# Performance work log

Hardware: AMD Instinct MI355X
Metric: run time of the kernel (lower is better)

## Reference

```python
import jax, jax.numpy as jnp
import numpy as np

N1 = 8000   # solute nodes
N2 = 8000   # solvent nodes
E = 128000  # edges per graph side (avg degree 16)
B = 128     # number of graphs in the batch
NFEAT, NHID, NCLS = 128, 256, 512
D = 2 * NCLS   # Set2Set input dim (1024)
H = D          # LSTM hidden = input_dim in DGL Set2Set


def setup_inputs() -> dict:
    key = jax.random.key(0)
    ks = jax.random.split(key, 24)
    w = lambda k, shp, fan: (jax.random.normal(k, shp, jnp.float32) / np.sqrt(fan))
    inp = {}
    inp["x1"] = jax.random.normal(ks[0], (N1, NFEAT), jnp.float32)
    inp["x2"] = jax.random.normal(ks[1], (N2, NFEAT), jnp.float32)
    inp["src1"] = jax.random.randint(ks[2], (E,), 0, N1, jnp.int32)
    inp["dst1"] = jax.random.randint(ks[3], (E,), 0, N1, jnp.int32)
    inp["src2"] = jax.random.randint(ks[4], (E,), 0, N2, jnp.int32)
    inp["dst2"] = jax.random.randint(ks[5], (E,), 0, N2, jnp.int32)
    inp["gid1"] = jnp.sort(jax.random.randint(ks[6], (N1,), 0, B, jnp.int32))
    inp["gid2"] = jnp.sort(jax.random.randint(ks[7], (N2,), 0, B, jnp.int32))
    # GraphConv weights (DGL stores W as [in, out]) + biases
    inp["W_gc1"] = w(ks[8], (NFEAT, NHID), NFEAT); inp["b_gc1"] = jnp.zeros((NHID,), jnp.float32)
    inp["W_gc2"] = w(ks[9], (NHID, NCLS), NHID);   inp["b_gc2"] = jnp.zeros((NCLS,), jnp.float32)
    inp["W_gc3"] = w(ks[10], (NFEAT, NHID), NFEAT); inp["b_gc3"] = jnp.zeros((NHID,), jnp.float32)
    inp["W_gc4"] = w(ks[11], (NHID, NCLS), NHID);   inp["b_gc4"] = jnp.zeros((NCLS,), jnp.float32)
    # Set2Set LSTM (input = 2*D, hidden = H), torch gate order i,f,g,o
    inp["W_ih"] = w(ks[12], (4 * H, 2 * D), 2 * D)
    inp["W_hh"] = w(ks[13], (4 * H, H), H)
    inp["b_ih"] = jnp.zeros((4 * H,), jnp.float32)
    inp["b_hh"] = jnp.zeros((4 * H,), jnp.float32)
    # MLP head
    inp["W_fc1"] = w(ks[14], (1024, 4096), 4096); inp["b_fc1"] = jnp.zeros((1024,), jnp.float32)
    inp["W_fc2"] = w(ks[15], (512, 1024), 1024);  inp["b_fc2"] = jnp.zeros((512,), jnp.float32)
    inp["W_fc3"] = w(ks[16], (1, 512), 512);      inp["b_fc3"] = jnp.zeros((1,), jnp.float32)
    return inp


def _gconv(x, src, dst, W, b, n):
    # DGL GraphConv, norm='both': D_out^{-1/2} scaling at src, sum over in-edges, D_in^{-1/2} at dst
    ones = jnp.ones(src.shape[0], x.dtype)
    outd = jnp.clip(jax.ops.segment_sum(ones, src, num_segments=n), 1.0)
    ind = jnp.clip(jax.ops.segment_sum(ones, dst, num_segments=n), 1.0)
    h = (x * (outd ** -0.5)[:, None]) @ W
    agg = jax.ops.segment_sum(h[src], dst, num_segments=n)   # sparse neighbor aggregation
    return agg * (ind ** -0.5)[:, None] + b


def _set2set(x, gid, Wih, Whh, bih, bhh):
    # DGL Set2Set, n_iters=2, 1-layer LSTM; x: [N, D], gid: [N] graph membership
    d = x.shape[1]
    q_star = jnp.zeros((B, 2 * d), x.dtype)
    h = jnp.zeros((B, d), x.dtype)
    c = jnp.zeros((B, d), x.dtype)
    for _ in range(2):
        gates = q_star @ Wih.T + h @ Whh.T + bih + bhh
        i, f, g, o = jnp.split(gates, 4, axis=1)
        c = jax.nn.sigmoid(f) * c + jax.nn.sigmoid(i) * jnp.tanh(g)
        h = jax.nn.sigmoid(o) * jnp.tanh(c)
        e = jnp.sum(x * h[gid], axis=1)                       # per-node attention logit
        m = jax.ops.segment_max(e, gid, num_segments=B)
        ex = jnp.exp(e - m[gid])
        s = jax.ops.segment_sum(ex, gid, num_segments=B)
        alpha = ex / s[gid]                                   # segment softmax
        r = jax.ops.segment_sum(alpha[:, None] * x, gid, num_segments=B)
        q_star = jnp.concatenate([h, r], axis=1)
    return q_star


def reference(x1, x2, src1, dst1, src2, dst2, gid1, gid2,
              W_gc1, b_gc1, W_gc2, b_gc2, W_gc3, b_gc3, W_gc4, b_gc4,
              W_ih, W_hh, b_ih, b_hh,
              W_fc1, b_fc1, W_fc2, b_fc2, W_fc3, b_fc3):
    s = jax.nn.relu(_gconv(x1, src1, dst1, W_gc1, b_gc1, N1))
    s = _gconv(s, src1, dst1, W_gc2, b_gc2, N1)
    v = jax.nn.relu(_gconv(x2, src2, dst2, W_gc3, b_gc3, N2))
    v = _gconv(v, src2, dst2, W_gc4, b_gc4, N2)
    # len_map = len1.T @ len2 == same-graph indicator for binary membership matrices
    len_map = (gid1[:, None] == gid2[None, :]).astype(s.dtype)
    imap = jnp.tanh(s @ v.T) * len_map                        # [N1, N2]
    solvent_prime = imap.T @ s                                # [N2, NCLS]
    solute_prime = imap @ v                                   # [N1, NCLS]
    sf = jnp.concatenate([s, solute_prime], axis=1)           # [N1, 2*NCLS]
    vf = jnp.concatenate([v, solvent_prime], axis=1)
    ss = _set2set(sf, gid1, W_ih, W_hh, b_ih, b_hh)           # [B, 4*NCLS]
    vs = _set2set(vf, gid2, W_ih, W_hh, b_ih, b_hh)
    z = jnp.concatenate([ss, vs], axis=1)                     # [B, 4096]
    z = jax.nn.relu(z @ W_fc1.T + b_fc1)
    z = jax.nn.relu(z @ W_fc2.T + b_fc2)
    return z @ W_fc3.T + b_fc3                                # [B, 1]
```

## Files before the change

### kernel.cpp

```cpp
#include <hip/hip_runtime.h>

#define DEV __device__ __forceinline__

typedef _Float16 half8 __attribute__((ext_vector_type(8)));
typedef _Float16 half4_t __attribute__((ext_vector_type(4)));
typedef float f32x4 __attribute__((ext_vector_type(4)));

DEV float ftanh(float x){
  float ax = fabsf(x);
  float e = __expf(-2.f*ax);
  float t = (1.f - e)/(1.f + e);
  return x < 0.f ? -t : t;
}
DEV float fsigm(float x){ return 1.f/(1.f + expf(-x)); }
DEV float wredsum(float v){
  #pragma unroll
  for (int o=32;o;o>>=1) v += __shfl_xor(v,o,64);
  return v;
}
DEV f32x4 MF(half8 a, half8 b, f32x4 c){
  return __builtin_amdgcn_mfma_f32_16x16x32_f16(a,b,c,0,0,0);
}
DEV void split8(float4 a0, float4 a1, half8& h, half8& l){
  float f[8] = {a0.x,a0.y,a0.z,a0.w,a1.x,a1.y,a1.z,a1.w};
  #pragma unroll
  for (int e=0;e<8;++e){
    _Float16 hh = (_Float16)f[e];
    h[e] = hh;
    l[e] = (_Float16)(f[e] - (float)hh);
  }
}

__global__ void k_zero_i32(int* __restrict__ p, int n){
  int i = blockIdx.x*256 + threadIdx.x; if (i<n) p[i]=0;
}

__global__ void k_hist2(const int* __restrict__ s1, const int* __restrict__ d1, int E1,
                        int* __restrict__ co1, int* __restrict__ ci1,
                        const int* __restrict__ s2, const int* __restrict__ d2, int E2,
                        int* __restrict__ co2, int* __restrict__ ci2){
  int e = blockIdx.x*256 + threadIdx.x;
  if (e < E1){ atomicAdd(&co1[s1[e]],1); atomicAdd(&ci1[d1[e]],1); }
  int f = e - E1;
  if (f >= 0 && f < E2){ atomicAdd(&co2[s2[f]],1); atomicAdd(&ci2[d2[f]],1); }
}

__global__ void k_scan2(const int* __restrict__ c1, int n1, int* __restrict__ r1,
                        const int* __restrict__ c2, int n2, int* __restrict__ r2){
  __shared__ int sm[1024];
  const int* cnt = blockIdx.x ? c2 : c1;
  int*       row = blockIdx.x ? r2 : r1;
  int n          = blockIdx.x ? n2 : n1;
  int t = threadIdx.x;
  int per = n/1024 + 1;
  int st = t*per;
  int s = 0;
  for (int i=st;i<st+per;++i) if (i<n) s += cnt[i];
  sm[t]=s; __syncthreads();
  for (int o=1;o<1024;o<<=1){
    int v = (t>=o)? sm[t-o]:0;
    __syncthreads();
    sm[t] += v;
    __syncthreads();
  }
  int base = sm[t]-s;
  for (int i=st;i<st+per;++i){
    if (i<=n) row[i]=base;
    if (i<n) base += cnt[i];
  }
}

__global__ void k_scale2(const int* __restrict__ co1, const int* __restrict__ ci1, int n1,
                         float* __restrict__ os1, float* __restrict__ is1,
                         const int* __restrict__ co2, const int* __restrict__ ci2, int n2,
                         float* __restrict__ os2, float* __restrict__ is2){
  int i = blockIdx.x*256+threadIdx.x;
  if (i<n1){
    int a = co1[i] > 1 ? co1[i] : 1;
    int b = ci1[i] > 1 ? ci1[i] : 1;
    os1[i] = 1.f/sqrtf((float)a);
    is1[i] = 1.f/sqrtf((float)b);
  }
  int j = i - n1;
  if (j>=0 && j<n2){
    int a = co2[j] > 1 ? co2[j] : 1;
    int b = ci2[j] > 1 ? ci2[j] : 1;
    os2[j] = 1.f/sqrtf((float)a);
    is2[j] = 1.f/sqrtf((float)b);
  }
}

__global__ void k_scatter2(const int* __restrict__ s1, const int* __restrict__ d1, int E1,
                           const int* __restrict__ row1, int* __restrict__ cur1, int* __restrict__ csr1,
                           const int* __restrict__ s2, const int* __restrict__ d2, int E2,
                           const int* __restrict__ row2, int* __restrict__ cur2, int* __restrict__ csr2){
  int e = blockIdx.x*256+threadIdx.x;
  if (e<E1){ int d=d1[e]; int p=atomicAdd(&cur1[d],1); csr1[row1[d]+p]=s1[e]; }
  int f = e - E1;
  if (f>=0 && f<E2){ int d=d2[f]; int p=atomicAdd(&cur2[d],1); csr2[row2[d]+p]=s2[f]; }
}

__global__ void k_goff2(const int* __restrict__ g1, int n1, int* __restrict__ o1,
                        const int* __restrict__ g2, int n2, int* __restrict__ o2, int B,
                        int* __restrict__ pb1, int* __restrict__ gm1,
                        int* __restrict__ pb2, int* __restrict__ gm2){
  __shared__ int sc[2][256];
  int t = threadIdx.x;
  const int* gid = (t>=256)? g2 : g1;
  int*      goff = (t>=256)? o2 : o1;
  int n          = (t>=256)? n2 : n1;
  const int side = t>>8, q = t & 255;
  if (q<=B){
    int lo=0, hi=n;
    while (lo<hi){ int mid=(lo+hi)>>1; if (gid[mid]<q) lo=mid+1; else hi=mid; }
    goff[q]=lo;
  }
  __syncthreads();
  int pc = 0;
  if (q < B){
    const int* go = side ? o2 : o1;
    int c = go[q+1]-go[q]; if (c>128) c=128;
    pc = (c+31)&~31;
  }
  sc[side][q] = pc;
  __syncthreads();
  for (int o=1;o<B;o<<=1){
    int v = (q>=o && q<B) ? sc[side][q-o] : 0;
    __syncthreads();
    if (q<B) sc[side][q] += v;
    __syncthreads();
  }
  if (q < B){
    int incl = sc[side][q];
    int pbv  = incl - pc;
    int* pb = side ? pb2 : pb1;
    int* gm = side ? gm2 : gm1;
    pb[q] = pbv;
    if (q == B-1) pb[B] = incl;
    int nb = pc>>5, b0 = pbv>>5;
    for (int k=0;k<nb;++k) gm[b0+k] = q;
  }
}

__global__ void k_agg_h(const float* __restrict__ x, int ldx, const float* __restrict__ osc,
                        const int* __restrict__ row, const int* __restrict__ csr,
                        _Float16* __restrict__ oh, _Float16* __restrict__ ol, int n, int f4shift){
  int F4 = 1<<f4shift;
  int node = blockIdx.x*(256>>f4shift) + (threadIdx.x>>f4shift);
  if (node>=n) return;
  int fc = threadIdx.x & (F4-1);
  int F = F4<<2;
  int rs=row[node], re=row[node+1];
  float ax=0, ay=0, az=0, aw=0;
  if (osc){
    for (int e=rs;e<re;++e){
      int s = csr[e];
      float sc = osc[s];
      const float4 v = *(const float4*)(x + (size_t)s*ldx + (fc<<2));
      ax += sc*v.x; ay += sc*v.y; az += sc*v.z; aw += sc*v.w;
    }
  } else {
    int e = rs;
    for (; e+1<re; e+=2){
      int s0 = csr[e], s1 = csr[e+1];
      const float4 v0 = *(const float4*)(x + (size_t)s0*ldx + (fc<<2));
      const float4 v1 = *(const float4*)(x + (size_t)s1*ldx + (fc<<2));
      ax += v0.x+v1.x; ay += v0.y+v1.y; az += v0.z+v1.z; aw += v0.w+v1.w;
    }
    if (e<re){
      int s0 = csr[e];
      const float4 v0 = *(const float4*)(x + (size_t)s0*ldx + (fc<<2));
      ax += v0.x; ay += v0.y; az += v0.z; aw += v0.w;
    }
  }
  half4_t hv, lv;
  hv.x = (_Float16)ax; lv.x = (_Float16)(ax - (float)hv.x);
  hv.y = (_Float16)ay; lv.y = (_Float16)(ay - (float)hv.y);
  hv.z = (_Float16)az; lv.z = (_Float16)(az - (float)hv.z);
  hv.w = (_Float16)aw; lv.w = (_Float16)(aw - (float)hv.w);
  size_t o = (size_t)node*F + (fc<<2);
  *(half4_t*)(oh + o) = hv;
  *(half4_t*)(ol + o) = lv;
}

__global__ void k_wpack4(const float* __restrict__ W0, const float* __restrict__ W1,
                         const float* __restrict__ W2, const float* __restrict__ W3,
                         _Float16* __restrict__ h0, _Float16* __restrict__ l0,
                         _Float16* __restrict__ h1, _Float16* __restrict__ l1,
                         _Float16* __restrict__ h2, _Float16* __restrict__ l2,
                         _Float16* __restrict__ h3, _Float16* __restrict__ l3){
  int w = blockIdx.y;
  const float* W = (w==0)?W0:(w==1)?W1:(w==2)?W2:W3;
  _Float16* oh = (w==0)?h0:(w==1)?h1:(w==2)?h2:h3;
  _Float16* ol = (w==0)?l0:(w==1)?l1:(w==2)?l2:l3;
  int K   = (w&1)? 256 : 128;
  int nsh = (w&1)? 9 : 8;
  int i = blockIdx.x*256 + threadIdx.x;
  if (i >= (K<<nsh)) return;
  int k = i >> nsh, n = i & ((1<<nsh)-1);
  float v = W[i];
  _Float16 h = (_Float16)v;
  _Float16 l = (_Float16)(v - (float)h);
  size_t p = (((size_t)(k>>3)<<nsh) + n)*8 + (k&7);
  oh[p] = h; ol[p] = l;
}

__global__ __launch_bounds__(256)
void k_wpackT(const float* __restrict__ W, int ldw, int N,
              _Float16* __restrict__ Bh, _Float16* __restrict__ Bl){
  __shared__ float st[32][260];
  const int k0 = (int)blockIdx.x << 8;
  const int n0 = (int)blockIdx.y << 5;
  const int t = threadIdx.x;
  const int r = t >> 3, la = t & 7;
  const float* src = W + (size_t)(n0 + r)*ldw + k0;
  #pragma unroll
  for (int q=0;q<8;++q){
    int f = (la<<2) + (q<<5);
    *(float4*)&st[r][f] = *(const float4*)(src + f);
  }
  __syncthreads();
  const int nl = t & 31;
  #pragma unroll
  for (int j=0;j<4;++j){
    int kbl = (t>>5) + (j<<3);
    half8 h8, l8;
    #pragma unroll
    for (int e=0;e<8;++e){
      float v = st[nl][(kbl<<3)+e];
      _Float16 hh = (_Float16)v;
      h8[e]=hh; l8[e]=(_Float16)(v-(float)hh);
    }
    size_t a = ((size_t)((k0>>3)+kbl)*N + n0 + nl)*8;
    *(half8*)(Bh + a) = h8;
    *(half8*)(Bl + a) = l8;
  }
}

__global__ __launch_bounds__(256)
void k_gconv_mfma(const _Float16* __restrict__ Ah0, const _Float16* __restrict__ Al0,
                  const _Float16* __restrict__ Ah1, const _Float16* __restrict__ Al1,
                  const _Float16* __restrict__ Bh0, const _Float16* __restrict__ Bl0,
                  const _Float16* __restrict__ Bh1, const _Float16* __restrict__ Bl1,
                  float* __restrict__ C0, float* __restrict__ C1, int ldc,
                  int M0, int M1, int N, int K,
                  const float* __restrict__ rs0, const float* __restrict__ rs1,
                  const float* __restrict__ bi0, const float* __restrict__ bi1, int relu,
                  const float* __restrict__ po0, const float* __restrict__ po1)
{
  __shared__ __align__(16) _Float16 Ahs[2][4096];
  __shared__ __align__(16) _Float16 Als[2][4096];

  const int gx = gridDim.x, gxy = gridDim.x*gridDim.y;
  const int nwg = gxy*2;
  int fid = blockIdx.x + gx*blockIdx.y + gxy*blockIdx.z;
  int q = nwg>>3, r = nwg&7;
  int xcd = fid & 7, idx = fid >> 3;
  int sid = (xcd<r ? xcd*(q+1) : r*(q+1)+(xcd-r)*q) + idx;
  const int z  = sid / gxy;  int rem = sid - z*gxy;
  const int by = rem / gx,  bx = rem - by*gx;

  const _Float16* Ah = z ? Ah1 : Ah0;
  const _Float16* Al = z ? Al1 : Al0;
  const _Float16* Bh = z ? Bh1 : Bh0;
  const _Float16* Bl = z ? Bl1 : Bl0;
  float*       C  = z ? C1 : C0;
  const float* rsc = z ? rs1 : rs0;
  const float* bia = z ? bi1 : bi0;
  const float* po  = z ? po1 : po0;
  const int M = z ? M1 : M0;

  const int row0 = by << 7;
  const int col0 = bx << 7;
  if (row0 >= ((M+127)&~127)) return;

  const int tid = threadIdx.x;
  const int am  = tid >> 2;
  const int akb = tid & 3;
  const int wid = tid >> 6, lane = tid & 63;
  const int wr = wid >> 1, wc = wid & 1;
  const int lr = lane & 15, lg = lane >> 4;

  f32x4 acc[4][4] = {};
  const int nt = K >> 5;
  const size_t rowK64 = (size_t)64 * K;
  const _Float16* Aph = Ah + (size_t)(row0 + am) * K + (akb<<3);
  const _Float16* Apl = Al + (size_t)(row0 + am) * K + (akb<<3);

  half8 gh0 = *(const half8*)(Aph);
  half8 gh1 = *(const half8*)(Aph + rowK64);
  half8 gl0 = *(const half8*)(Apl);
  half8 gl1 = *(const half8*)(Apl + rowK64);
  *(half8*)&Ahs[0][(akb*128 + am)*8]      = gh0;
  *(half8*)&Ahs[0][(akb*128 + am + 64)*8] = gh1;
  *(half8*)&Als[0][(akb*128 + am)*8]      = gl0;
  *(half8*)&Als[0][(akb*128 + am + 64)*8] = gl1;
  __syncthreads();

  for (int c = 0; c < nt; ++c){
    const int cb = c & 1;
    if (c + 1 < nt){
      const int k0 = (c + 1) << 5;
      gh0 = *(const half8*)(Aph + k0);
      gh1 = *(const half8*)(Aph + k0 + rowK64);
      gl0 = *(const half8*)(Apl + k0);
      gl1 = *(const half8*)(Apl + k0 + rowK64);
    }
    const size_t kb0 = (size_t)(c<<2) + lg;
    half8 bh[4], bl[4];
    #pragma unroll
    for (int ni=0;ni<4;++ni){
      size_t a = (kb0*N + col0 + (wc<<6) + (ni<<4) + lr)*8;
      bh[ni] = *(const half8*)(Bh + a);
      bl[ni] = *(const half8*)(Bl + a);
    }
    #pragma unroll
    for (int mi=0;mi<4;++mi){
      const int aa = ((lg<<7) + (wr<<6) + (mi<<4) + lr)<<3;
      half8 ah = *(const half8*)&Ahs[cb][aa];
      half8 al = *(const half8*)&Als[cb][aa];
      #pragma unroll
      for (int ni=0;ni<4;++ni){
        acc[mi][ni] = MF(ah, bh[ni], acc[mi][ni]);
        acc[mi][ni] = MF(al, bh[ni], acc[mi][ni]);
        acc[mi][ni] = MF(ah, bl[ni], acc[mi][ni]);
      }
    }
    if (c + 1 < nt){
      const int nb_ = cb ^ 1;
      *(half8*)&Ahs[nb_][(akb*128 + am)*8]      = gh0;
      *(half8*)&Ahs[nb_][(akb*128 + am + 64)*8] = gh1;
      *(half8*)&Als[nb_][(akb*128 + am)*8]      = gl0;
      *(half8*)&Als[nb_][(akb*128 + am + 64)*8] = gl1;
    }
    __syncthreads();
  }

  #pragma unroll
  for (int ni = 0; ni < 4; ++ni){
    int cc = col0 + (wc<<6) + (ni<<4) + lr;
    float bv = bia ? bia[cc] : 0.f;
    #pragma unroll
    for (int mi = 0; mi < 4; ++mi){
      int rbase = row0 + (wr<<6) + (mi<<4) + (lg<<2);
      #pragma unroll
      for (int j = 0; j < 4; ++j){
        int rr = rbase + j;
        if (rr < M){
          float rs_ = rsc ? rsc[rr] : 1.f;
          float v = acc[mi][ni][j]*rs_ + bv;
          if (relu) v = fmaxf(v, 0.f);
          if (po) v *= po[rr];
          C[(size_t)rr*ldc + cc] = v;
        }
      }
    }
  }
}

__global__ __launch_bounds__(256)
void k_pack(const float* __restrict__ sf, const float* __restrict__ vf,
            const int* __restrict__ go1, const int* __restrict__ go2,
            const int* __restrict__ pb1, const int* __restrict__ pb2,
            const int* __restrict__ gm1, const int* __restrict__ gm2,
            _Float16* __restrict__ p1h, _Float16* __restrict__ p1l,
            _Float16* __restrict__ p2h, _Float16* __restrict__ p2l, int B)
{
  __shared__ float st[32][516];
  const int side = blockIdx.y;
  const float* x = side ? vf : sf;
  const int* go = side ? go2 : go1;
  const int* pb = side ? pb2 : pb1;
  const int* gm = side ? gm2 : gm1;
  _Float16* ph = side ? p2h : p1h;
  _Float16* pl = side ? p2l : p1l;
  const int u = blockIdx.x;
  if (u*32 >= pb[B]) return;
  const int g = gm[u];
  const int j0 = u*32 - pb[g];
  const int base = go[g];
  int cnt = go[g+1]-base; if (cnt>128) cnt=128;
  const int t = threadIdx.x;
  const int r = t>>3, f0 = (t&7)<<2;
  const bool valid = (j0 + r) < cnt;
  const float* src = x + (size_t)(base + j0 + r)*1024;
  #pragma unroll
  for (int q=0;q<16;++q){
    int f = f0 + (q<<5);
    float4 vv;
    if (valid) vv = *(const float4*)(src + f);
    else { vv.x=0.f; vv.y=0.f; vv.z=0.f; vv.w=0.f; }
    *(float4*)&st[r][f] = vv;
  }
  __syncthreads();
  #pragma unroll
  for (int q=0;q<8;++q){
    int u2 = t + (q<<8);
    int jg = u2>>9, f = u2&511;
    half8 h8, l8;
    #pragma unroll
    for (int e=0;e<8;++e){
      float vvv = st[(jg<<3)+e][f];
      _Float16 hh = (_Float16)vvv;
      h8[e]=hh; l8[e]=(_Float16)(vvv-(float)hh);
    }
    size_t a = ((size_t)((u<<2)+jg)<<12) + ((size_t)f<<3);
    *(half8*)(ph + a) = h8;
    *(half8*)(pl + a) = l8;
  }
}

__global__ __launch_bounds__(256)
void k_T(const float* __restrict__ sf, const float* __restrict__ vf,
         const int* __restrict__ go1, const int* __restrict__ go2,
         _Float16* __restrict__ Th, _Float16* __restrict__ Tl, int B)
{
  __shared__ __align__(16) _Float16 Ahs[64*136 + 8];
  __shared__ __align__(16) _Float16 Als[64*136 + 8];
  __shared__ __align__(16) _Float16 Bhs[2][2048];
  __shared__ __align__(16) _Float16 Bls[2][2048];
  const int g = blockIdx.x, rt = blockIdx.y;
  int gR = go1[g]; int c1 = go1[g+1]-gR; if (c1>128) c1=128;
  int gO = go2[g]; int c2 = go2[g+1]-gO; if (c2>128) c2=128;
  const int c1_32 = (c1+31)&~31, c2_32 = (c2+31)&~31;
  if ((rt<<4) >= c1_32 || c2_32 == 0) return;
  const int tid = threadIdx.x;
  {
    const int r = tid >> 4;
    const int f0 = (tid & 15) << 5;
    const int row = (rt<<4) + r;
    const bool val = row < c1;
    const float* src = sf + (size_t)(gR + row)*1024 + f0;
    #pragma unroll
    for (int q=0;q<4;++q){
      float4 v0, v1;
      if (val){
        v0 = *(const float4*)(src + (q<<3));
        v1 = *(const float4*)(src + (q<<3) + 4);
      } else {
        v0.x=0.f; v0.y=0.f; v0.z=0.f; v0.w=0.f; v1 = v0;
      }
      half8 h,l; split8(v0,v1,h,l);
      const int a = ((f0>>3) + q)*136 + (r<<3);
      *(half8*)&Ahs[a] = h; *(half8*)&Als[a] = l;
    }
  }
  const int w = tid>>6, lane = tid&63, lr = lane&15, lg = lane>>4;
  const int bc = tid>>2, bfg = tid&3, bf = bfg<<3;
  const int bwr = (bfg<<9) + ((bc ^ (bfg<<2))<<3);
  const int ncc = (c2_32 + 63) >> 6;
  _Float16* T0h = Th + ((size_t)g<<14);
  _Float16* T0l = Tl + ((size_t)g<<14);
  _Float16* T1h = Th + ((size_t)(B + g)<<14);
  _Float16* T1l = Tl + ((size_t)(B + g)<<14);
  for (int cc=0; cc<ncc; ++cc){
    const int cbase = cc<<6;
    const int colr = cbase + bc;
    const bool bval = colr < c2;
    const float* bsrc = vf + (size_t)(gO + colr)*1024 + bf;
    {
      float4 v0, v1;
      if (bval){ v0 = *(const float4*)(bsrc); v1 = *(const float4*)(bsrc + 4); }
      else { v0.x=0.f; v0.y=0.f; v0.z=0.f; v0.w=0.f; v1 = v0; }
      half8 h,l; split8(v0,v1,h,l);
      *(half8*)&Bhs[0][bwr] = h; *(half8*)&Bls[0][bwr] = l;
    }
    __syncthreads();
    f32x4 acc = {0.f,0.f,0.f,0.f};
    const int col_l = (w<<4) + lr;
    const int ba = (lg<<9) + ((col_l ^ (lg<<2))<<3);
    for (int kc=0; kc<16; ++kc){
      float4 p0, p1;
      if (kc+1<16){
        if (bval){
          const float* s = bsrc + ((kc+1)<<5);
          p0 = *(const float4*)s; p1 = *(const float4*)(s + 4);
        } else { p0.x=0.f; p0.y=0.f; p0.z=0.f; p0.w=0.f; p1 = p0; }
      }
      const int aa = ((kc<<2)+lg)*136 + (lr<<3);
      half8 ah = *(const half8*)&Ahs[aa];
      half8 al = *(const half8*)&Als[aa];
      half8 bh = *(const half8*)&Bhs[kc&1][ba];
      half8 bl = *(const half8*)&Bls[kc&1][ba];
      acc = MF(ah,bh,acc);
      acc = MF(al,bh,acc);
      acc = MF(ah,bl,acc);
      if (kc+1<16){
        half8 h,l; split8(p0,p1,h,l);
        *(half8*)&Bhs[(kc+1)&1][bwr] = h; *(half8*)&Bls[(kc+1)&1][bwr] = l;
      }
      __syncthreads();
    }
    const int col = cbase + col_l;
    if (col < c2_32){
      half4_t t1h, t1l;
      #pragma unroll
      for (int qq=0;qq<4;++qq){
        int r = (rt<<4) + (lg<<2) + qq;
        float t = (r < c1 && col < c2) ? ftanh(acc[qq]) : 0.f;
        _Float16 hh = (_Float16)t;
        _Float16 ll = (_Float16)(t - (float)hh);
        T0h[(r<<7) + col] = hh;
        T0l[(r<<7) + col] = ll;
        t1h[qq] = hh; t1l[qq] = ll;
      }
      const int r0 = (rt<<4) + (lg<<2);
      *(half4_t*)&T1h[(col<<7) + r0] = t1h;
      *(half4_t*)&T1l[(col<<7) + r0] = t1l;
    }
  }
}

__global__ __launch_bounds__(256)
void k_apply(const _Float16* __restrict__ Th, const _Float16* __restrict__ Tl,
             const _Float16* __restrict__ p1h, const _Float16* __restrict__ p1l,
             const _Float16* __restrict__ p2h, const _Float16* __restrict__ p2l,
             const int* __restrict__ go1, const int* __restrict__ go2,
             const int* __restrict__ pb1, const int* __restrict__ pb2,
             float* __restrict__ sf, float* __restrict__ vf, int B)
{
  const int side = blockIdx.x, g = blockIdx.y, ft = blockIdx.z;
  const int* goR = side ? go2 : go1;
  const int* goO = side ? go1 : go2;
  const int* pbO = side ? pb1 : pb2;
  const _Float16* oph = side ? p1h : p2h;
  const _Float16* opl = side ? p1l : p2l;
  float* outp = side ? vf : sf;
  int gR = goR[g]; int cR = goR[g+1]-gR; if (cR>128) cR=128;
  int gO = goO[g]; int cO = goO[g+1]-gO; if (cO>128) cO=128;
  if (cR <= 0) return;
  const int pO = pbO[g];
  const int cO32 = (cO+31)&~31;
  const int MR = ((cR+15)&~15)>>4;
  const _Float16* Tph = Th + ((size_t)(side*B + g)<<14);
  const _Float16* Tpl = Tl + ((size_t)(side*B + g)<<14);
  const int tid = threadIdx.x, w = tid>>6, lane = tid&63;
  const int lr = lane&15, lg = lane>>4;
  const int f0 = (ft<<8) + (w<<6);
  for (int rc = 0; rc < MR; rc += 4){
    f32x4 acc[4][4];
    #pragma unroll
    for (int a_=0;a_<4;++a_)
      #pragma unroll
      for (int b_=0;b_<4;++b_) acc[a_][b_] = (f32x4){0.f,0.f,0.f,0.f};
    for (int k0=0; k0<cO32; k0+=32){
      half8 bh[4], bl[4];
      #pragma unroll
      for (int nj=0;nj<4;++nj){
        size_t a = ((size_t)((pO + k0)>>3) + lg)*4096 + (size_t)(f0 + (nj<<4) + lr)*8;
        bh[nj] = *(const half8*)(oph + a);
        bl[nj] = *(const half8*)(opl + a);
      }
      #pragma unroll
      for (int mi=0;mi<4;++mi){
        if (rc + mi < MR){
          int a = ((((rc+mi)<<4) + lr)<<7) + k0 + (lg<<3);
          half8 th_ = *(const half8*)&Tph[a];
          half8 tl_ = *(const half8*)&Tpl[a];
          #pragma unroll
          for (int nj=0;nj<4;++nj){
            acc[mi][nj] = MF(th_, bh[nj], acc[mi][nj]);
            acc[mi][nj] = MF(tl_, bh[nj], acc[mi][nj]);
            acc[mi][nj] = MF(th_, bl[nj], acc[mi][nj]);
          }
        }
      }
    }
    #pragma unroll
    for (int mi=0;mi<4;++mi){
      if (rc + mi < MR){
        #pragma unroll
        for (int nj=0;nj<4;++nj){
          #pragma unroll
          for (int qq=0;qq<4;++qq){
            int r = (((rc+mi)<<4)) + (lg<<2) + qq;
            if (r < cR)
              outp[(size_t)(gR + r)*1024 + 512 + f0 + (nj<<4) + lr] = acc[mi][nj][qq];
          }
        }
      }
    }
  }
}

__global__ __launch_bounds__(256)
void k_gemmsk(const float* __restrict__ Ab, size_t AsideOff, int lda,
              const float* __restrict__ Bm, int ldb,
              float* __restrict__ P, int M, int N, int kchunk)
{
  __shared__ float As[2][16][132];
  __shared__ float Bs[2][16][68];
  const int tid = threadIdx.x;
  const int col0 = (int)blockIdx.x << 6;
  const int kbeg = (int)blockIdx.z * kchunk;
  const float* A = Ab + (size_t)blockIdx.y * AsideOff;
  const int ar = tid >> 1, ak = (tid & 1) << 3;
  const int br = tid >> 2, bk = (tid & 3) << 2;
  const int tx = tid & 15, ty = tid >> 4;
  const float* Arow = A + (size_t)ar * lda + kbeg + ak;
  const float* Brow = Bm + (size_t)(col0 + br) * ldb + kbeg + bk;
  float acc[8][4] = {};
  float4 a0 = *(const float4*)(Arow);
  float4 a1 = *(const float4*)(Arow + 4);
  float4 b0 = *(const float4*)(Brow);
  As[0][ak+0][ar]=a0.x; As[0][ak+1][ar]=a0.y; As[0][ak+2][ar]=a0.z; As[0][ak+3][ar]=a0.w;
  As[0][ak+4][ar]=a1.x; As[0][ak+5][ar]=a1.y; As[0][ak+6][ar]=a1.z; As[0][ak+7][ar]=a1.w;
  Bs[0][bk+0][br]=b0.x; Bs[0][bk+1][br]=b0.y; Bs[0][bk+2][br]=b0.z; Bs[0][bk+3][br]=b0.w;
  __syncthreads();
  const int nt = kchunk >> 4;
  for (int t = 0; t < nt; ++t){
    const int cb = t & 1;
    if (t + 1 < nt){
      int k0 = (t + 1) << 4;
      a0 = *(const float4*)(Arow + k0);
      a1 = *(const float4*)(Arow + k0 + 4);
      b0 = *(const float4*)(Brow + k0);
    }
    #pragma unroll
    for (int kk = 0; kk < 16; ++kk){
      float4 b4 = *(const float4*)&Bs[cb][kk][tx << 2];
      float4 a4 = *(const float4*)&As[cb][kk][ty << 3];
      float4 a5 = *(const float4*)&As[cb][kk][(ty << 3) + 4];
      acc[0][0]+=a4.x*b4.x; acc[0][1]+=a4.x*b4.y; acc[0][2]+=a4.x*b4.z; acc[0][3]+=a4.x*b4.w;
      acc[1][0]+=a4.y*b4.x; acc[1][1]+=a4.y*b4.y; acc[1][2]+=a4.y*b4.z; acc[1][3]+=a4.y*b4.w;
      acc[2][0]+=a4.z*b4.x; acc[2][1]+=a4.z*b4.y; acc[2][2]+=a4.z*b4.z; acc[2][3]+=a4.z*b4.w;
      acc[3][0]+=a4.w*b4.x; acc[3][1]+=a4.w*b4.y; acc[3][2]+=a4.w*b4.z; acc[3][3]+=a4.w*b4.w;
      acc[4][0]+=a5.x*b4.x; acc[4][1]+=a5.x*b4.y; acc[4][2]+=a5.x*b4.z; acc[4][3]+=a5.x*b4.w;
      acc[5][0]+=a5.y*b4.x; acc[5][1]+=a5.y*b4.y; acc[5][2]+=a5.y*b4.z; acc[5][3]+=a5.y*b4.w;
      acc[6][0]+=a5.z*b4.x; acc[6][1]+=a5.z*b4.y; acc[6][2]+=a5.z*b4.z; acc[6][3]+=a5.z*b4.w;
      acc[7][0]+=a5.w*b4.x; acc[7][1]+=a5.w*b4.y; acc[7][2]+=a5.w*b4.z; acc[7][3]+=a5.w*b4.w;
    }
    if (t + 1 < nt){
      const int nb = cb ^ 1;
      As[nb][ak+0][ar]=a0.x; As[nb][ak+1][ar]=a0.y; As[nb][ak+2][ar]=a0.z; As[nb][ak+3][ar]=a0.w;
      As[nb][ak+4][ar]=a1.x; As[nb][ak+5][ar]=a1.y; As[nb][ak+6][ar]=a1.z; As[nb][ak+7][ar]=a1.w;
      Bs[nb][bk+0][br]=b0.x; Bs[nb][bk+1][br]=b0.y; Bs[nb][bk+2][br]=b0.z; Bs[nb][bk+3][br]=b0.w;
    }
    __syncthreads();
  }
  float* Pz = P + (size_t)(blockIdx.y*gridDim.z + blockIdx.z) * M * N;
  #pragma unroll
  for (int i = 0; i < 8; ++i){
    int rr = (ty << 3) + i;
    float4 v = {acc[i][0], acc[i][1], acc[i][2], acc[i][3]};
    *(float4*)(Pz + (size_t)rr*N + col0 + (tx<<2)) = v;
  }
}

__global__ __launch_bounds__(256)
void k_gemmsk_h(const float* __restrict__ Ab, size_t AsideOff, int lda,
                const _Float16* __restrict__ Bhp, const _Float16* __restrict__ Blp,
                float* __restrict__ P, int N, int kchunk)
{
  __shared__ __align__(16) _Float16 Ahs[2][4096];
  __shared__ __align__(16) _Float16 Als[2][4096];
  const int tid = threadIdx.x;
  const int col0 = (int)blockIdx.x << 7;
  const int kbeg = (int)blockIdx.z * kchunk;
  const float* A = Ab + (size_t)blockIdx.y * AsideOff;
  const int ar = tid >> 1, aq = (tid & 1) << 4;
  const int wid = tid>>6, lane = tid&63;
  const int wr = wid>>1, wc = wid&1;
  const int lr = lane&15, lg = lane>>4;
  const float* Arow = A + (size_t)ar*lda + kbeg + aq;
  const int akb = aq>>3;
  f32x4 acc[4][4] = {};
  const int nc = kchunk >> 5;
  float4 g0,g1,g2,g3;
  g0 = *(const float4*)(Arow);     g1 = *(const float4*)(Arow+4);
  g2 = *(const float4*)(Arow+8);   g3 = *(const float4*)(Arow+12);
  {
    half8 h,l;
    split8(g0,g1,h,l);
    *(half8*)&Ahs[0][(akb*128+ar)*8] = h;     *(half8*)&Als[0][(akb*128+ar)*8] = l;
    split8(g2,g3,h,l);
    *(half8*)&Ahs[0][((akb+1)*128+ar)*8] = h; *(half8*)&Als[0][((akb+1)*128+ar)*8] = l;
  }
  __syncthreads();
  for (int c=0;c<nc;++c){
    const int cb = c&1;
    if (c+1<nc){
      const float* p = Arow + ((c+1)<<5);
      g0 = *(const float4*)(p);    g1 = *(const float4*)(p+4);
      g2 = *(const float4*)(p+8);  g3 = *(const float4*)(p+12);
    }
    const size_t kb0 = (size_t)((kbeg + (c<<5)) >> 3) + lg;
    half8 bh[4], bl[4];
    #pragma unroll
    for (int ni=0;ni<4;++ni){
      size_t a = (kb0*N + col0 + (wc<<6) + (ni<<4) + lr)*8;
      bh[ni] = *(const half8*)(Bhp + a);
      bl[ni] = *(const half8*)(Blp + a);
    }
    #pragma unroll
    for (int mi=0;mi<4;++mi){
      int aa = ((lg<<7) + (wr<<6) + (mi<<4) + lr)<<3;
      half8 ah = *(const half8*)&Ahs[cb][aa];
      half8 al = *(const half8*)&Als[cb][aa];
      #pragma unroll
      for (int ni=0;ni<4;++ni){
        acc[mi][ni] = MF(ah,bh[ni],acc[mi][ni]);
        acc[mi][ni] = MF(al,bh[ni],acc[mi][ni]);
        acc[mi][ni] = MF(ah,bl[ni],acc[mi][ni]);
      }
    }
    if (c+1<nc){
      const int nb = cb^1;
      half8 h,l;
      split8(g0,g1,h,l);
      *(half8*)&Ahs[nb][(akb*128+ar)*8] = h;     *(half8*)&Als[nb][(akb*128+ar)*8] = l;
      split8(g2,g3,h,l);
      *(half8*)&Ahs[nb][((akb+1)*128+ar)*8] = h; *(half8*)&Als[nb][((akb+1)*128+ar)*8] = l;
    }
    __syncthreads();
  }
  float* Pz = P + (size_t)(blockIdx.y*gridDim.z + blockIdx.z)*128*N;
  #pragma unroll
  for (int mi=0;mi<4;++mi){
    #pragma unroll
    for (int ni=0;ni<4;++ni){
      int cc2 = col0 + (wc<<6) + (ni<<4) + lr;
      #pragma unroll
      for (int j=0;j<4;++j){
        int rr2 = (wr<<6) + (mi<<4) + (lg<<2) + j;
        Pz[(size_t)rr2*N + cc2] = acc[mi][ni][j];
      }
    }
  }
}

__global__ void k_red_bias(const float* __restrict__ P, int split, int MN, int N,
                           const float* __restrict__ bias, float* __restrict__ C, int relu){
  int i = blockIdx.x*256 + threadIdx.x;
  if (i >= MN) return;
  float v = bias[i & (N-1)];
  for (int s=0;s<split;++s) v += P[(size_t)s*MN + i];
  if (relu) v = fmaxf(v, 0.f);
  C[i] = v;
}

__global__ void k_lstm1(const float* __restrict__ bih, const float* __restrict__ bhh,
                        float* __restrict__ c1, float* __restrict__ h1){
  int j = blockIdx.x*256 + threadIdx.x;
  if (j >= 1024) return;
  float gi = bih[j]        + bhh[j];
  float gg = bih[j+2048]   + bhh[j+2048];
  float go = bih[j+3072]   + bhh[j+3072];
  float cc = fsigm(gi)*ftanh(gg);
  c1[j] = cc;
  h1[j] = fsigm(go)*ftanh(cc);
}

__global__ void k_gemv_u(const float* __restrict__ Wih, const float* __restrict__ Whh,
                         const float* __restrict__ bih, const float* __restrict__ bhh,
                         const float* __restrict__ h1, float* __restrict__ u){
  int w = (blockIdx.x*256 + threadIdx.x)>>6;
  int lane = threadIdx.x & 63;
  if (w >= 4096) return;
  const float* wi = Wih + (size_t)w*2048;
  const float* wh = Whh + (size_t)w*1024;
  float acc = 0.f;
  #pragma unroll
  for (int qq=0;qq<4;++qq){
    int o = qq*256 + (lane<<2);
    float4 hv = *(const float4*)(h1 + o);
    float4 a  = *(const float4*)(wi + o);
    float4 b  = *(const float4*)(wh + o);
    acc += hv.x*(a.x+b.x) + hv.y*(a.y+b.y) + hv.z*(a.z+b.z) + hv.w*(a.w+b.w);
  }
  acc = wredsum(acc);
  if (lane==0) u[w] = acc + bih[w] + bhh[w];
}

__global__ __launch_bounds__(256)
void k_attn(const float* __restrict__ sf, const float* __restrict__ vf,
            const int* __restrict__ go1, const int* __restrict__ go2,
            const float* __restrict__ hbase, size_t hSideOff, int hstride,
            float* __restrict__ outbase, size_t oSideOff, int ldout)
{
  __shared__ float hs[1024];
  __shared__ float ech[1024];
  __shared__ float red[8];
  int side = blockIdx.y;
  const float* x = side? vf : sf;
  const int* goff = side? go2 : go1;
  const float* hsrc = hbase + (size_t)side*hSideOff;
  float* outp = outbase + (size_t)side*oSideOff;
  int b = blockIdx.x, t = threadIdx.x;
  int i0 = goff[b], i1 = goff[b+1];
  int lane = t & 63, wv = t >> 6;
  { float4 hv = *(const float4*)(hsrc + (size_t)b*hstride + (t<<2));
    *(float4*)&hs[t<<2] = hv; }
  __syncthreads();
  float m = -3.0e38f, s = 0.f;
  float ax=0, ay=0, az=0, aw=0;
  for (int c = i0; c < i1; c += 1024){
    int ce = c + 1024; if (ce > i1) ce = i1;
    int n = ce - c;
    float wmax = -3.0e38f;
    for (int i = c + wv; i < ce; i += 4){
      const float* xr = x + (size_t)i*1024;
      float d = 0.f;
      #pragma unroll
      for (int qq=0;qq<4;++qq){
        int o = qq*256 + (lane<<2);
        float4 xv = *(const float4*)(xr+o);
        float4 h4 = *(const float4*)&hs[o];
        d += xv.x*h4.x + xv.y*h4.y + xv.z*h4.z + xv.w*h4.w;
      }
      d = wredsum(d);
      if (lane==0) ech[i-c] = d;
      wmax = fmaxf(wmax, d);
    }
    if (lane==0) red[wv] = wmax;
    __syncthreads();
    float cm = fmaxf(fmaxf(red[0],red[1]), fmaxf(red[2],red[3]));
    float nm = fmaxf(m, cm);
    float scale = __expf(m - nm);
    s *= scale; ax*=scale; ay*=scale; az*=scale; aw*=scale;
    float ps = 0.f;
    for (int k = t; k < n; k += 256) ps += __expf(ech[k]-nm);
    ps = wredsum(ps);
    __syncthreads();
    if (lane==0) red[wv] = ps;
    __syncthreads();
    s += red[0]+red[1]+red[2]+red[3];
    for (int k = 0; k < n; ++k){
      float w = __expf(ech[k]-nm);
      float4 xv = *(const float4*)(x + (size_t)(c+k)*1024 + (t<<2));
      ax += w*xv.x; ay += w*xv.y; az += w*xv.z; aw += w*xv.w;
    }
    m = nm;
    __syncthreads();
  }
  float inv = (i1>i0 && s>0.f) ? 1.f/s : 0.f;
  float4 o = {ax*inv, ay*inv, az*inv, aw*inv};
  *(float4*)(outp + (size_t)b*ldout + (t<<2)) = o;
}

__global__ void k_lstm2_red(const float* __restrict__ Pb, size_t PsideOff, int split,
                            const float* __restrict__ u, const float* __restrict__ c1,
                            float* __restrict__ z, int B){
  int idx = blockIdx.x*256 + threadIdx.x;
  if (idx >= B*1024) return;
  int side = blockIdx.y;
  const float* P = Pb + (size_t)side*PsideOff;
  int b = idx >> 10, j = idx & 1023;
  float gi=u[j], gf=u[j+1024], gg=u[j+2048], go=u[j+3072];
  const float* g = P + (size_t)b*4096;
  for (int s=0;s<split;++s){
    const float* gs = g + (size_t)s*B*4096;
    gi += gs[j]; gf += gs[j+1024]; gg += gs[j+2048]; go += gs[j+3072];
  }
  float cc = fsigm(gf)*c1[j] + fsigm(gi)*ftanh(gg);
  z[(size_t)b*4096 + side*2048 + j] = fsigm(go)*ftanh(cc);
}

__global__ void k_fc3(const float* __restrict__ z2, const float* __restrict__ w3,
                      const float* __restrict__ b3, float* __restrict__ out, int B){
  int wv = (blockIdx.x*256+threadIdx.x)>>6;
  int lane = threadIdx.x & 63;
  if (wv >= B) return;
  const float* zr = z2 + (size_t)wv*512;
  float acc=0.f;
  #pragma unroll
  for (int qq=0;qq<2;++qq){
    int o = qq*256 + (lane<<2);
    float4 a  = *(const float4*)(zr + o);
    float4 ww = *(const float4*)(w3 + o);
    acc += a.x*ww.x + a.y*ww.y + a.z*ww.z + a.w*ww.w;
  }
  acc = wredsum(acc);
  if (lane==0) out[wv] = acc + b3[0];
}

extern "C" void kernel_launch(void* const* d_in, const int* in_sizes, int n_in,
                              void* d_out, int out_size, void* d_ws, size_t ws_size,
                              hipStream_t stream)
{
  const float* x1  = (const float*)d_in[0];
  const float* x2  = (const float*)d_in[1];
  const int* src1  = (const int*)d_in[2];
  const int* dst1  = (const int*)d_in[3];
  const int* src2  = (const int*)d_in[4];
  const int* dst2  = (const int*)d_in[5];
  const int* gid1  = (const int*)d_in[6];
  const int* gid2  = (const int*)d_in[7];
  const float* Wg1 = (const float*)d_in[8];  const float* bg1 = (const float*)d_in[9];
  const float* Wg2 = (const float*)d_in[10]; const float* bg2 = (const float*)d_in[11];
  const float* Wg3 = (const float*)d_in[12]; const float* bg3 = (const float*)d_in[13];
  const float* Wg4 = (const float*)d_in[14]; const float* bg4 = (const float*)d_in[15];
  const float* Wih = (const float*)d_in[16]; const float* Whh = (const float*)d_in[17];
  const float* bih = (const float*)d_in[18]; const float* bhh = (const float*)d_in[19];
  const float* Wf1 = (const float*)d_in[20]; const float* bf1 = (const float*)d_in[21];
  const float* Wf2 = (const float*)d_in[22]; const float* bf2 = (const float*)d_in[23];
  const float* Wf3 = (const float*)d_in[24]; const float* bf3 = (const float*)d_in[25];
  float* out = (float*)d_out;

  const int N1 = in_sizes[0]/128;
  const int N2 = in_sizes[1]/128;
  const int E1 = in_sizes[2];
  const int E2 = in_sizes[4];
  const int B  = out_size;
  const int NM = N1>N2?N1:N2;

  char* base = (char*)d_ws; size_t off=0;
  auto alloc = [&](size_t bytes)->void*{ void* p = base+off; off += (bytes+255)&~(size_t)255; return p; };

  int* zr   = (int*)alloc(sizeof(int)*(size_t)(3*N1+3*N2));
  int* co1=zr, *ci1=zr+N1, *cur1=zr+2*N1;
  int* co2=zr+3*N1, *ci2=zr+3*N1+N2, *cur2=zr+3*N1+2*N2;
  int* row1 = (int*)alloc(sizeof(int)*(size_t)(N1+1));
  int* row2 = (int*)alloc(sizeof(int)*(size_t)(N2+1));
  int* csr1 = (int*)alloc(sizeof(int)*(size_t)E1);
  int* csr2 = (int*)alloc(sizeof(int)*(size_t)E2);
  int* go1  = (int*)alloc(sizeof(int)*(size_t)(B+1));
  int* go2  = (int*)alloc(sizeof(int)*(size_t)(B+1));
  int* pb1  = (int*)alloc(sizeof(int)*(size_t)(B+1));
  int* pb2  = (int*)alloc(sizeof(int)*(size_t)(B+1));
  int* gm1  = (int*)alloc(sizeof(int)*1024);
  int* gm2  = (int*)alloc(sizeof(int)*1024);
  float* os1 = (float*)alloc(sizeof(float)*(size_t)N1);
  float* is1 = (float*)alloc(sizeof(float)*(size_t)N1);
  float* os2 = (float*)alloc(sizeof(float)*(size_t)N2);
  float* is2 = (float*)alloc(sizeof(float)*(size_t)N2);
  _Float16* a1h = (_Float16*)alloc(sizeof(_Float16)*(size_t)(NM+128)*256);
  _Float16* a1l = (_Float16*)alloc(sizeof(_Float16)*(size_t)(NM+128)*256);
  _Float16* a2h = (_Float16*)alloc(sizeof(_Float16)*(size_t)(NM+128)*256);
  _Float16* a2l = (_Float16*)alloc(sizeof(_Float16)*(size_t)(NM+128)*256);
  _Float16* wg1h = (_Float16*)alloc(sizeof(_Float16)*32768);
  _Float16* wg1l = (_Float16*)alloc(sizeof(_Float16)*32768);
  _Float16* wg2h = (_Float16*)alloc(sizeof(_Float16)*131072);
  _Float16* wg2l = (_Float16*)alloc(sizeof(_Float16)*131072);
  _Float16* wg3h = (_Float16*)alloc(sizeof(_Float16)*32768);
  _Float16* wg3l = (_Float16*)alloc(sizeof(_Float16)*32768);
  _Float16* wg4h = (_Float16*)alloc(sizeof(_Float16)*131072);
  _Float16* wg4l = (_Float16*)alloc(sizeof(_Float16)*131072);
  _Float16* wihh = (_Float16*)alloc(sizeof(_Float16)*(size_t)4096*1024);
  _Float16* wihl = (_Float16*)alloc(sizeof(_Float16)*(size_t)4096*1024);
  _Float16* wf1h = (_Float16*)alloc(sizeof(_Float16)*(size_t)1024*4096);
  _Float16* wf1l = (_Float16*)alloc(sizeof(_Float16)*(size_t)1024*4096);
  float* sf  = (float*)alloc(sizeof(float)*(size_t)(N1+128)*1024);
  float* vf  = (float*)alloc(sizeof(float)*(size_t)(N2+128)*1024);
  float* h1 = (float*)alloc(sizeof(float)*1024);
  float* c1 = (float*)alloc(sizeof(float)*1024);
  float* u  = (float*)alloc(sizeof(float)*4096);
  float* r1 = (float*)alloc(sizeof(float)*(size_t)2*B*1024);
  float* z1 = (float*)alloc(sizeof(float)*(size_t)B*1024);
  float* z2 = (float*)alloc(sizeof(float)*(size_t)B*512);
  float* z  = (float*)alloc(sizeof(float)*(size_t)B*4096);
  _Float16* Tqh = (_Float16*)alloc(sizeof(_Float16)*(size_t)2*B*16384);
  _Float16* Tql = (_Float16*)alloc(sizeof(_Float16)*(size_t)2*B*16384);
  const int PN = ((NM + 32*B + 63)&~63) + 64;
  const size_t PE = (size_t)PN*512;
  size_t packedBytes = 4*PE*sizeof(_Float16);
  size_t pbufBytes   = sizeof(float)*(size_t)32*B*1024*4;
  char* uni = (char*)alloc(packedBytes > pbufBytes ? packedBytes : pbufBytes);
  _Float16* p1h = (_Float16*)uni;
  _Float16* p1l = p1h + PE;
  _Float16* p2h = p1l + PE;
  _Float16* p2l = p2h + PE;
  float* Pbuf = (float*)uni;
  if (off > ws_size) return;

  float* hb1 = sf + 512;
  float* hb2 = vf + 512;

  dim3 blk(256);

  k_wpack4<<<dim3(512,4),blk,0,stream>>>(Wg1,Wg2,Wg3,Wg4,
                                         wg1h,wg1l, wg2h,wg2l, wg3h,wg3l, wg4h,wg4l);
  k_wpackT<<<dim3(4,128),blk,0,stream>>>(Wih+1024, 2048, 4096, wihh, wihl);
  k_wpackT<<<dim3(16,32),blk,0,stream>>>(Wf1, 4096, 1024, wf1h, wf1l);

  k_zero_i32<<<(3*N1+3*N2+255)/256, blk, 0, stream>>>(zr, 3*N1+3*N2);
  k_hist2<<<(E1+E2+255)/256, blk, 0, stream>>>(src1,dst1,E1,co1,ci1, src2,dst2,E2,co2,ci2);
  k_scan2<<<2,1024,0,stream>>>(ci1,N1,row1, ci2,N2,row2);
  k_scale2<<<(N1+N2+255)/256,blk,0,stream>>>(co1,ci1,N1,os1,is1, co2,ci2,N2,os2,is2);
  k_scatter2<<<(E1+E2+255)/256,blk,0,stream>>>(src1,dst1,E1,row1,cur1,csr1, src2,dst2,E2,row2,cur2,csr2);
  k_goff2<<<1,512,0,stream>>>(gid1,N1,go1, gid2,N2,go2, B, pb1,gm1, pb2,gm2);

  int gy = (NM+127)/128;
  k_agg_h<<<(N1+7)/8,blk,0,stream>>>(x1,128, os1,row1,csr1, a1h,a1l, N1,5);
  k_agg_h<<<(N2+7)/8,blk,0,stream>>>(x2,128, os2,row2,csr2, a2h,a2l, N2,5);
  k_gconv_mfma<<<dim3(2,gy,2),blk,0,stream>>>(a1h,a1l, a2h,a2l,
                                              wg1h,wg1l, wg3h,wg3l,
                                              hb1,hb2,1024, N1,N2, 256,128,
                                              is1,is2, bg1,bg3, 1, os1,os2);
  k_agg_h<<<(N1+3)/4,blk,0,stream>>>(hb1,1024, nullptr,row1,csr1, a1h,a1l, N1,6);
  k_agg_h<<<(N2+3)/4,blk,0,stream>>>(hb2,1024, nullptr,row2,csr2, a2h,a2l, N2,6);
  k_gconv_mfma<<<dim3(4,gy,2),blk,0,stream>>>(a1h,a1l, a2h,a2l,
                                              wg2h,wg2l, wg4h,wg4l,
                                              sf,vf,1024, N1,N2, 512,256,
                                              is1,is2, bg2,bg4, 0, nullptr,nullptr);

  const int GMAX = NM/32 + B + 2;
  k_pack<<<dim3(GMAX,2),blk,0,stream>>>(sf,vf, go1,go2, pb1,pb2, gm1,gm2,
                                        p1h,p1l, p2h,p2l, B);
  k_T<<<dim3(B,8),blk,0,stream>>>(sf,vf, go1,go2, Tqh,Tql, B);
  k_apply<<<dim3(2,B,2),blk,0,stream>>>(Tqh,Tql, p1h,p1l, p2h,p2l,
                                        go1,go2, pb1,pb2, sf,vf, B);

  k_lstm1<<<4,blk,0,stream>>>(bih,bhh,c1,h1);
  k_gemv_u<<<1024,blk,0,stream>>>(Wih,Whh,bih,bhh,h1,u);

  k_attn<<<dim3(B,2),blk,0,stream>>>(sf,vf,go1,go2, h1,0,0, r1,(size_t)B*1024,1024);
  k_gemmsk_h<<<dim3(32,2,4),blk,0,stream>>>(r1,(size_t)B*1024,1024, wihh,wihl, Pbuf, 4096,256);
  k_lstm2_red<<<dim3((B*1024+255)/256,2),blk,0,stream>>>(Pbuf,(size_t)4*B*4096,4, u,c1, z,B);
  k_attn<<<dim3(B,2),blk,0,stream>>>(sf,vf,go1,go2, z,2048,4096, z+1024,2048,4096);

  k_gemmsk_h<<<dim3(8,1,32),blk,0,stream>>>(z,0,4096, wf1h,wf1l, Pbuf, 1024,128);
  k_red_bias<<<(B*1024+255)/256,blk,0,stream>>>(Pbuf,32,B*1024,1024,bf1,z1,1);
  k_gemmsk<<<dim3(8,1,8),blk,0,stream>>>(z1,0,1024, Wf2,1024, Pbuf, 128,512,128);
  k_red_bias<<<(B*512+255)/256,blk,0,stream>>>(Pbuf,8,B*512,512,bf2,z2,1);
  k_fc3<<<(B*64+255)/256,blk,0,stream>>>(z2,Wf3,bf3,out,B);
}
```

Measured before the change: 381.4 us.

## Single-pass online-softmax attention and fuse LSTM step-1 into GEMV kernel

The Set2Set attention kernel now does one pass per wave, keeping a running max, running sum and a rescaled accumulator, and merges the four wave partials through shared memory at the end. This replaces the old chunked scheme that read each node row twice and synchronised several times per chunk. The first LSTM step (computed from biases only) moves into the GEMV kernel, and the reducer recomputes c1 from the biases, which removes one launch and the c1 buffer. In exchange, every GEMV block redundantly evaluates the 1024 gate activations, and each wave serialises over its own rows with branchy rescaling.

```diff
diff --git a/kernel.cpp b/kernel.cpp
--- a/kernel.cpp
+++ b/kernel.cpp
@@ -739,23 +739,24 @@
   C[i] = v;
 }
 
-__global__ void k_lstm1(const float* __restrict__ bih, const float* __restrict__ bhh,
-                        float* __restrict__ c1, float* __restrict__ h1){
-  int j = blockIdx.x*256 + threadIdx.x;
-  if (j >= 1024) return;
-  float gi = bih[j]        + bhh[j];
-  float gg = bih[j+2048]   + bhh[j+2048];
-  float go = bih[j+3072]   + bhh[j+3072];
-  float cc = fsigm(gi)*ftanh(gg);
-  c1[j] = cc;
-  h1[j] = fsigm(go)*ftanh(cc);
-}
-
 __global__ void k_gemv_u(const float* __restrict__ Wih, const float* __restrict__ Whh,
                          const float* __restrict__ bih, const float* __restrict__ bhh,
-                         const float* __restrict__ h1, float* __restrict__ u){
-  int w = (blockIdx.x*256 + threadIdx.x)>>6;
-  int lane = threadIdx.x & 63;
+                         float* __restrict__ h1, float* __restrict__ u){
+  __shared__ float hsv[1024];
+  int t = threadIdx.x;
+  #pragma unroll
+  for (int j=t; j<1024; j+=256){
+    float gi = bih[j]        + bhh[j];
+    float gg = bih[j+2048]   + bhh[j+2048];
+    float go = bih[j+3072]   + bhh[j+3072];
+    float cc = fsigm(gi)*ftanh(gg);
+    float hv = fsigm(go)*ftanh(cc);
+    hsv[j] = hv;
+    if (blockIdx.x==0) h1[j] = hv;
+  }
+  __syncthreads();
+  int w = (blockIdx.x*256 + t)>>6;
+  int lane = t & 63;
   if (w >= 4096) return;
   const float* wi = Wih + (size_t)w*2048;
   const float* wh = Whh + (size_t)w*1024;
@@ -763,7 +764,7 @@
   #pragma unroll
   for (int qq=0;qq<4;++qq){
     int o = qq*256 + (lane<<2);
-    float4 hv = *(const float4*)(h1 + o);
+    float4 hv = *(const float4*)&hsv[o];
     float4 a  = *(const float4*)(wi + o);
     float4 b  = *(const float4*)(wh + o);
     acc += hv.x*(a.x+b.x) + hv.y*(a.y+b.y) + hv.z*(a.z+b.z) + hv.w*(a.w+b.w);
@@ -779,8 +780,8 @@
             float* __restrict__ outbase, size_t oSideOff, int ldout)
 {
   __shared__ float hs[1024];
-  __shared__ float ech[1024];
-  __shared__ float red[8];
+  __shared__ float part[4][1024];
+  __shared__ float redm[4], reds[4];
   int side = blockIdx.y;
   const float* x = side? vf : sf;
   const int* goff = side? go2 : go1;
@@ -793,53 +794,74 @@
     *(float4*)&hs[t<<2] = hv; }
   __syncthreads();
   float m = -3.0e38f, s = 0.f;
-  float ax=0, ay=0, az=0, aw=0;
-  for (int c = i0; c < i1; c += 1024){
-    int ce = c + 1024; if (ce > i1) ce = i1;
-    int n = ce - c;
-    float wmax = -3.0e38f;
-    for (int i = c + wv; i < ce; i += 4){
-      const float* xr = x + (size_t)i*1024;
-      float d = 0.f;
+  float4 acc[4];
+  #pragma unroll
+  for (int qq=0;qq<4;++qq){ acc[qq].x=0.f; acc[qq].y=0.f; acc[qq].z=0.f; acc[qq].w=0.f; }
+  for (int i = i0 + wv; i < i1; i += 4){
+    const float* xr = x + (size_t)i*1024;
+    float4 xv[4];
+    float d = 0.f;
+    #pragma unroll
+    for (int qq=0;qq<4;++qq){
+      int o = qq*256 + (lane<<2);
+      xv[qq] = *(const float4*)(xr+o);
+      float4 h4 = *(const float4*)&hs[o];
+      d += xv[qq].x*h4.x + xv[qq].y*h4.y + xv[qq].z*h4.z + xv[qq].w*h4.w;
+    }
+    d = wredsum(d);
+    if (d > m){
+      float sc = __expf(m - d);
+      s = s*sc + 1.f;
       #pragma unroll
       for (int qq=0;qq<4;++qq){
-        int o = qq*256 + (lane<<2);
-        float4 xv = *(const float4*)(xr+o);
-        float4 h4 = *(const float4*)&hs[o];
-        d += xv.x*h4.x + xv.y*h4.y + xv.z*h4.z + xv.w*h4.w;
-      }
-      d = wredsum(d);
-      if (lane==0) ech[i-c] = d;
-      wmax = fmaxf(wmax, d);
-    }
-    if (lane==0) red[wv] = wmax;
-    __syncthreads();
-    float cm = fmaxf(fmaxf(red[0],red[1]), fmaxf(red[2],red[3]));
-    float nm = fmaxf(m, cm);
-    float scale = __expf(m - nm);
-    s *= scale; ax*=scale; ay*=scale; az*=scale; aw*=scale;
-    float ps = 0.f;
-    for (int k = t; k < n; k += 256) ps += __expf(ech[k]-nm);
-    ps = wredsum(ps);
-    __syncthreads();
-    if (lane==0) red[wv] = ps;
-    __syncthreads();
-    s += red[0]+red[1]+red[2]+red[3];
-    for (int k = 0; k < n; ++k){
-      float w = __expf(ech[k]-nm);
-      float4 xv = *(const float4*)(x + (size_t)(c+k)*1024 + (t<<2));
-      ax += w*xv.x; ay += w*xv.y; az += w*xv.z; aw += w*xv.w;
-    }
-    m = nm;
-    __syncthreads();
-  }
-  float inv = (i1>i0 && s>0.f) ? 1.f/s : 0.f;
-  float4 o = {ax*inv, ay*inv, az*inv, aw*inv};
-  *(float4*)(outp + (size_t)b*ldout + (t<<2)) = o;
+        acc[qq].x = acc[qq].x*sc + xv[qq].x;
+        acc[qq].y = acc[qq].y*sc + xv[qq].y;
+        acc[qq].z = acc[qq].z*sc + xv[qq].z;
+        acc[qq].w = acc[qq].w*sc + xv[qq].w;
+      }
+      m = d;
+    } else {
+      float ww = __expf(d - m);
+      s += ww;
+      #pragma unroll
+      for (int qq=0;qq<4;++qq){
+        acc[qq].x += ww*xv[qq].x;
+        acc[qq].y += ww*xv[qq].y;
+        acc[qq].z += ww*xv[qq].z;
+        acc[qq].w += ww*xv[qq].w;
+      }
+    }
+  }
+  if (lane==0){ redm[wv]=m; reds[wv]=s; }
+  __syncthreads();
+  float gm = fmaxf(fmaxf(redm[0],redm[1]), fmaxf(redm[2],redm[3]));
+  float gs = reds[0]*__expf(redm[0]-gm) + reds[1]*__expf(redm[1]-gm)
+           + reds[2]*__expf(redm[2]-gm) + reds[3]*__expf(redm[3]-gm);
+  float wsc = __expf(m - gm);
+  #pragma unroll
+  for (int qq=0;qq<4;++qq){
+    float4 v = acc[qq];
+    v.x*=wsc; v.y*=wsc; v.z*=wsc; v.w*=wsc;
+    *(float4*)&part[wv][qq*256 + (lane<<2)] = v;
+  }
+  __syncthreads();
+  float inv = (i1>i0 && gs>0.f) ? 1.f/gs : 0.f;
+  int col = t<<2;
+  float4 p0 = *(float4*)&part[0][col];
+  float4 p1 = *(float4*)&part[1][col];
+  float4 p2 = *(float4*)&part[2][col];
+  float4 p3 = *(float4*)&part[3][col];
+  float4 o;
+  o.x = (p0.x+p1.x+p2.x+p3.x)*inv;
+  o.y = (p0.y+p1.y+p2.y+p3.y)*inv;
+  o.z = (p0.z+p1.z+p2.z+p3.z)*inv;
+  o.w = (p0.w+p1.w+p2.w+p3.w)*inv;
+  *(float4*)(outp + (size_t)b*ldout + col) = o;
 }
 
 __global__ void k_lstm2_red(const float* __restrict__ Pb, size_t PsideOff, int split,
-                            const float* __restrict__ u, const float* __restrict__ c1,
+                            const float* __restrict__ u,
+                            const float* __restrict__ bih, const float* __restrict__ bhh,
                             float* __restrict__ z, int B){
   int idx = blockIdx.x*256 + threadIdx.x;
   if (idx >= B*1024) return;
@@ -852,7 +874,10 @@
     const float* gs = g + (size_t)s*B*4096;
     gi += gs[j]; gf += gs[j+1024]; gg += gs[j+2048]; go += gs[j+3072];
   }
-  float cc = fsigm(gf)*c1[j] + fsigm(gi)*ftanh(gg);
+  float b_i = bih[j] + bhh[j];
+  float b_g = bih[j+2048] + bhh[j+2048];
+  float c1v = fsigm(b_i)*ftanh(b_g);
+  float cc = fsigm(gf)*c1v + fsigm(gi)*ftanh(gg);
   z[(size_t)b*4096 + side*2048 + j] = fsigm(go)*ftanh(cc);
 }
 
@@ -943,7 +968,6 @@
   float* sf  = (float*)alloc(sizeof(float)*(size_t)(N1+128)*1024);
   float* vf  = (float*)alloc(sizeof(float)*(size_t)(N2+128)*1024);
   float* h1 = (float*)alloc(sizeof(float)*1024);
-  float* c1 = (float*)alloc(sizeof(float)*1024);
   float* u  = (float*)alloc(sizeof(float)*4096);
   float* r1 = (float*)alloc(sizeof(float)*(size_t)2*B*1024);
   float* z1 = (float*)alloc(sizeof(float)*(size_t)B*1024);
@@ -1001,12 +1025,11 @@
   k_apply<<<dim3(2,B,2),blk,0,stream>>>(Tqh,Tql, p1h,p1l, p2h,p2l,
                                         go1,go2, pb1,pb2, sf,vf, B);
 
-  k_lstm1<<<4,blk,0,stream>>>(bih,bhh,c1,h1);
   k_gemv_u<<<1024,blk,0,stream>>>(Wih,Whh,bih,bhh,h1,u);
 
   k_attn<<<dim3(B,2),blk,0,stream>>>(sf,vf,go1,go2, h1,0,0, r1,(size_t)B*1024,1024);
   k_gemmsk_h<<<dim3(32,2,4),blk,0,stream>>>(r1,(size_t)B*1024,1024, wihh,wihl, Pbuf, 4096,256);
-  k_lstm2_red<<<dim3((B*1024+255)/256,2),blk,0,stream>>>(Pbuf,(size_t)4*B*4096,4, u,c1, z,B);
+  k_lstm2_red<<<dim3((B*1024+255)/256,2),blk,0,stream>>>(Pbuf,(size_t)4*B*4096,4, u, bih,bhh, z,B);
   k_attn<<<dim3(B,2),blk,0,stream>>>(sf,vf,go1,go2, z,2048,4096, z+1024,2048,4096);
 
   k_gemmsk_h<<<dim3(8,1,32),blk,0,stream>>>(z,0,4096, wf1h,wf1l, Pbuf, 1024,128);
```

Result: faster. 369.5 us (-3.1%).
